# Optimization experiments

Measured on AMD Instinct MI355X. Metric: run time of the kernel, lower is better.

## Reference

```python
import jax, jax.numpy as jnp
import numpy as np

NHEAD = 8
DMODEL = 512
DK = DMODEL // NHEAD  # 64

def setup_inputs() -> dict:
    key = jax.random.key(0)
    ks = jax.random.split(key, 7)
    B, S = 4, 2048
    Q = jax.random.normal(ks[0], (B, S, DMODEL), dtype=jnp.float32)
    K = jax.random.normal(ks[1], (B, S, DMODEL), dtype=jnp.float32)
    V = jax.random.normal(ks[2], (B, S, DMODEL), dtype=jnp.float32)
    # Original uses torch.rand (uniform [0,1)) for all weights.
    WQ = jax.random.uniform(ks[3], (NHEAD, DMODEL, DK), dtype=jnp.float32)
    WK = jax.random.uniform(ks[4], (NHEAD, DMODEL, DK), dtype=jnp.float32)
    WV = jax.random.uniform(ks[5], (NHEAD, DMODEL, DK), dtype=jnp.float32)
    WO = jax.random.uniform(ks[6], (NHEAD * DK, DMODEL), dtype=jnp.float32)
    return {"Q": Q, "K": K, "V": V, "WQ": WQ, "WK": WK, "WV": WV, "WO": WO}

def reference(Q, K, V, WQ, WK, WV, WO):
    # Stacked per-head projections: [B,H,S,dk]
    Qh = jnp.einsum('bsd,hdk->bhsk', Q, WQ)
    Kh = jnp.einsum('bsd,hdk->bhsk', K, WK)
    Vh = jnp.einsum('bsd,hdk->bhsk', V, WV)
    dk = Kh.shape[-1]
    scores = jnp.einsum('bhqk,bhsk->bhqs', Qh, Kh) / jnp.sqrt(jnp.float32(dk))
    attn = jax.nn.softmax(scores, axis=-1)  # dropout omitted (eval / deterministic baseline)
    out = jnp.einsum('bhqs,bhsk->bhqk', attn, Vh)
    B, H, S, Dk = out.shape
    out = out.transpose(0, 2, 1, 3).reshape(B, S, H * Dk)  # concat heads on last dim
    return out @ WO
```

## Files before the change

kernel.cpp:

```cpp
#include <hip/hip_runtime.h>

#define NB 4
#define NS 2048
#define ND 512
#define NH 8
#define NDK 64

typedef __attribute__((ext_vector_type(8))) short bf16x8;
typedef __attribute__((ext_vector_type(4))) short bf16x4;
typedef __attribute__((ext_vector_type(4))) float f32x4;
typedef __attribute__((ext_vector_type(4))) int   i32x4;

__device__ inline f32x4 mfma16(bf16x8 a, bf16x8 b, f32x4 c) {
    return __builtin_amdgcn_mfma_f32_16x16x32_bf16(a, b, c, 0, 0, 0);
}
__device__ inline unsigned short f2bf(float f) {
    unsigned u = __float_as_uint(f);
    unsigned r = u + 0x7FFFu + ((u >> 16) & 1u);
    return (unsigned short)(r >> 16);
}
__device__ inline float bf2f(unsigned short h) {
    return __uint_as_float(((unsigned)h) << 16);
}
__device__ inline void splitf(float x, short& hi, short& lo) {
    unsigned short h = f2bf(x);
    hi = (short)h;
    lo = (short)f2bf(x - bf2f(h));
}
__device__ inline float exp2_fast(float x) {
    float r; asm("v_exp_f32 %0, %1" : "=v"(r) : "v"(x)); return r;
}

__global__ __launch_bounds__(256) void prep_split(
    const float* __restrict__ X, short* __restrict__ xh, short* __restrict__ xl)
{
    int i = (blockIdx.x * 256 + threadIdx.x) * 4;
    float4 f = *(const float4*)(X + i);
    short h0,h1,h2,h3,l0,l1,l2,l3;
    splitf(f.x,h0,l0); splitf(f.y,h1,l1); splitf(f.z,h2,l2); splitf(f.w,h3,l3);
    bf16x4 hv = {h0,h1,h2,h3}, lv = {l0,l1,l2,l3};
    *(bf16x4*)(xh + i) = hv;
    *(bf16x4*)(xl + i) = lv;
}

__global__ __launch_bounds__(256) void proj_kernel(
    const short* __restrict__ xqh, const short* __restrict__ xql,
    const short* __restrict__ xkh, const short* __restrict__ xkl,
    const float* __restrict__ Vf,
    const float* __restrict__ WQ, const float* __restrict__ WK,
    const float* __restrict__ WV,
    short* __restrict__ qth, short* __restrict__ qtl,
    short* __restrict__ kth, short* __restrict__ ktl,
    short* __restrict__ vt, int zbase)
{
    const int z = zbase + blockIdx.z;
    const int m0 = blockIdx.x * 128;
    const int h  = blockIdx.y;
    const int tid = threadIdx.x;
    const int w = tid >> 6, lane = tid & 63, c = lane & 15, g = lane >> 4;

    const short* xh = (z == 0) ? xqh : xkh;
    const short* xl = (z == 0) ? xql : xkl;
    const float* Wp = ((z == 0) ? WQ : (z == 1) ? WK : WV) + (size_t)h * ND * NDK;
    short* o1 = (z == 0) ? qth : (z == 1) ? kth : vt;
    short* o2 = (z == 0) ? qtl : ktl;

    __shared__ __align__(16) short smem[15360];
    short* sxh = smem;
    short* sxl = smem + 5120;
    short* swh = smem + 10240;
    short* swl = smem + 12800;

    f32x4 acc[2][4];
    #pragma unroll
    for (int i = 0; i < 2; i++)
        #pragma unroll
        for (int j = 0; j < 4; j++) acc[i][j] = f32x4{0.f,0.f,0.f,0.f};

    const int r_ = tid >> 1, kq = (tid & 1) * 16;
    const int kr0 = (tid*2) >> 4,     c40 = ((tid*2) & 15) * 4;
    const int kr1 = (tid*2+1) >> 4,   c41 = ((tid*2+1) & 15) * 4;

    bf16x8 rh0, rh1, rl0, rl1;
    float4 rv0, rv1, rv2, rv3;
    float4 rw0, rw1;

    auto LDX = [&](int k0) {
        if (z < 2) {
            const short* s1 = xh + (size_t)(m0 + r_) * ND + k0 + kq;
            const short* s2 = xl + (size_t)(m0 + r_) * ND + k0 + kq;
            rh0 = *(const bf16x8*)s1; rh1 = *(const bf16x8*)(s1 + 8);
            rl0 = *(const bf16x8*)s2; rl1 = *(const bf16x8*)(s2 + 8);
        } else {
            const float* s1 = Vf + (size_t)(m0 + r_) * ND + k0 + kq;
            rv0 = ((const float4*)s1)[0]; rv1 = ((const float4*)s1)[1];
            rv2 = ((const float4*)s1)[2]; rv3 = ((const float4*)s1)[3];
        }
    };
    auto LDW = [&](int k0) {
        rw0 = *(const float4*)(Wp + (size_t)(k0 + kr0) * NDK + c40);
        rw1 = *(const float4*)(Wp + (size_t)(k0 + kr1) * NDK + c41);
    };

    LDX(0); LDW(0);

    for (int k0 = 0; k0 < ND; k0 += 32) {
        if (z < 2) {
            *(bf16x8*)&sxh[r_*40 + kq]     = rh0;
            *(bf16x8*)&sxh[r_*40 + kq + 8] = rh1;
            *(bf16x8*)&sxl[r_*40 + kq]     = rl0;
            *(bf16x8*)&sxl[r_*40 + kq + 8] = rl1;
            short hh, ll;
            splitf(rw0.x, hh, ll); swh[(c40+0)*40 + kr0] = hh; swl[(c40+0)*40 + kr0] = ll;
            splitf(rw0.y, hh, ll); swh[(c40+1)*40 + kr0] = hh; swl[(c40+1)*40 + kr0] = ll;
            splitf(rw0.z, hh, ll); swh[(c40+2)*40 + kr0] = hh; swl[(c40+2)*40 + kr0] = ll;
            splitf(rw0.w, hh, ll); swh[(c40+3)*40 + kr0] = hh; swl[(c40+3)*40 + kr0] = ll;
            splitf(rw1.x, hh, ll); swh[(c41+0)*40 + kr1] = hh; swl[(c41+0)*40 + kr1] = ll;
            splitf(rw1.y, hh, ll); swh[(c41+1)*40 + kr1] = hh; swl[(c41+1)*40 + kr1] = ll;
            splitf(rw1.z, hh, ll); swh[(c41+2)*40 + kr1] = hh; swl[(c41+2)*40 + kr1] = ll;
            splitf(rw1.w, hh, ll); swh[(c41+3)*40 + kr1] = hh; swl[(c41+3)*40 + kr1] = ll;
        } else {
            short tmp[16];
            tmp[0]=(short)f2bf(rv0.x); tmp[1]=(short)f2bf(rv0.y);
            tmp[2]=(short)f2bf(rv0.z); tmp[3]=(short)f2bf(rv0.w);
            tmp[4]=(short)f2bf(rv1.x); tmp[5]=(short)f2bf(rv1.y);
            tmp[6]=(short)f2bf(rv1.z); tmp[7]=(short)f2bf(rv1.w);
            tmp[8]=(short)f2bf(rv2.x); tmp[9]=(short)f2bf(rv2.y);
            tmp[10]=(short)f2bf(rv2.z); tmp[11]=(short)f2bf(rv2.w);
            tmp[12]=(short)f2bf(rv3.x); tmp[13]=(short)f2bf(rv3.y);
            tmp[14]=(short)f2bf(rv3.z); tmp[15]=(short)f2bf(rv3.w);
            bf16x8 v0, v1;
            #pragma unroll
            for (int j = 0; j < 8; j++) { v0[j] = tmp[j]; v1[j] = tmp[8+j]; }
            *(bf16x8*)&sxh[r_*40 + kq]     = v0;
            *(bf16x8*)&sxh[r_*40 + kq + 8] = v1;
            swh[(c40+0)*40 + kr0] = (short)f2bf(rw0.x);
            swh[(c40+1)*40 + kr0] = (short)f2bf(rw0.y);
            swh[(c40+2)*40 + kr0] = (short)f2bf(rw0.z);
            swh[(c40+3)*40 + kr0] = (short)f2bf(rw0.w);
            swh[(c41+0)*40 + kr1] = (short)f2bf(rw1.x);
            swh[(c41+1)*40 + kr1] = (short)f2bf(rw1.y);
            swh[(c41+2)*40 + kr1] = (short)f2bf(rw1.z);
            swh[(c41+3)*40 + kr1] = (short)f2bf(rw1.w);
        }
        __syncthreads();

        if (k0 + 32 < ND) { LDX(k0 + 32); LDW(k0 + 32); }

        bf16x8 ah0 = *(bf16x8*)&sxh[(32*w +      c)*40 + 8*g];
        bf16x8 ah1 = *(bf16x8*)&sxh[(32*w + 16 + c)*40 + 8*g];
        bf16x8 al0, al1;
        if (z < 2) {
            al0 = *(bf16x8*)&sxl[(32*w +      c)*40 + 8*g];
            al1 = *(bf16x8*)&sxl[(32*w + 16 + c)*40 + 8*g];
        }
        #pragma unroll
        for (int nf = 0; nf < 4; nf++) {
            bf16x8 bh = *(bf16x8*)&swh[(c + 16*nf)*40 + 8*g];
            acc[0][nf] = mfma16(ah0, bh, acc[0][nf]);
            acc[1][nf] = mfma16(ah1, bh, acc[1][nf]);
            if (z < 2) {
                bf16x8 bl = *(bf16x8*)&swl[(c + 16*nf)*40 + 8*g];
                acc[0][nf] = mfma16(ah0, bl, acc[0][nf]);
                acc[1][nf] = mfma16(ah1, bl, acc[1][nf]);
                acc[0][nf] = mfma16(al0, bh, acc[0][nf]);
                acc[1][nf] = mfma16(al1, bh, acc[1][nf]);
            }
        }
        __syncthreads();
    }

    const int bh = (m0 >> 11) * NH + h;
    if (z < 2) {
        short* ep = smem;
        #pragma unroll
        for (int pass = 0; pass < 2; pass++) {
            __syncthreads();
            #pragma unroll
            for (int mi = 0; mi < 2; mi++)
                #pragma unroll
                for (int nf = 0; nf < 4; nf++)
                    #pragma unroll
                    for (int r = 0; r < 4; r++) {
                        int rl = 32*w + 16*mi + 4*g + r;
                        short hh, ll; splitf(acc[mi][nf][r], hh, ll);
                        ep[rl*72 + c + 16*nf] = pass ? ll : hh;
                    }
            __syncthreads();
            int rl = tid >> 1, half = tid & 1;
            int s = (m0 & 2047) + rl;
            int t = s >> 6, sr = s & 63;
            char* op = (char*)(pass ? o2 : o1) + ((size_t)bh * 32 + t) * 8192 + sr * 128;
            int sw = (sr & 7) << 4;
            #pragma unroll
            for (int ch = 0; ch < 4; ch++) {
                bf16x8 vv = *(bf16x8*)&ep[rl*72 + half*32 + ch*8];
                *(bf16x8*)(op + ((half*64 + ch*16) ^ sw)) = vv;
            }
        }
    } else {
        short* ep = smem;
        __syncthreads();
        #pragma unroll
        for (int mi = 0; mi < 2; mi++)
            #pragma unroll
            for (int nf = 0; nf < 4; nf++)
                #pragma unroll
                for (int r = 0; r < 4; r++) {
                    int rl = 32*w + 16*mi + 4*g + r;
                    ep[rl*72 + c + 16*nf] = (short)f2bf(acc[mi][nf][r]);
                }
        __syncthreads();
        int dk = tid >> 2, scq = (tid & 3) * 32;
        #pragma unroll
        for (int ch = 0; ch < 4; ch++) {
            int sl = scq + ch*8;
            int s = (m0 & 2047) + sl;
            int t = s >> 6, sr0 = s & 63;
            bf16x8 vv;
            #pragma unroll
            for (int i = 0; i < 8; i++) vv[i] = ep[(sl + i)*72 + dk];
            char* op = (char*)o1 + ((size_t)bh * 32 + t) * 8192 + dk * 128;
            *(bf16x8*)(op + ((2*sr0) ^ ((dk & 7) << 4))) = vv;
        }
    }
}

__global__ __launch_bounds__(256, 4) void attn_kernel(
    const short* __restrict__ qth, const short* __restrict__ qtl,
    const short* __restrict__ kth, const short* __restrict__ ktl,
    const short* __restrict__ vtl, short* __restrict__ ao)
{
    const int orig = blockIdx.x;
    const int wg = (orig & 7) * 128 + (orig >> 3);
    const int bh = wg >> 5, qb = (wg & 31) * 64;
    const int tid = threadIdx.x;
    const int w = tid >> 6, lane = tid & 63, c = lane & 15, g = lane >> 4;

    __shared__ __align__(16) short kh_s[64*64];
    __shared__ __align__(16) short kl_s[64*64];
    __shared__ __align__(16) short v_s [64*64];
    __shared__ __align__(16) short pb  [4][16*64];
    char* khb = (char*)kh_s;
    char* klb = (char*)kl_s;
    char* vb  = (char*)v_s;
    char* pwb = (char*)pb[w];
    short* pw = pb[w];

    bf16x8 qh[2], ql[2];
    {
        const char* qtbh = (const char*)qth + ((size_t)bh*32 + (qb>>6))*8192;
        const char* qtbl = (const char*)qtl + ((size_t)bh*32 + (qb>>6))*8192;
        int s_in = 16*w + c;
        int sw = (s_in & 7) << 4;
        qh[0] = *(const bf16x8*)(qtbh + s_in*128 + ((16*g) ^ sw));
        qh[1] = *(const bf16x8*)(qtbh + s_in*128 + ((64 + 16*g) ^ sw));
        ql[0] = *(const bf16x8*)(qtbl + s_in*128 + ((16*g) ^ sw));
        ql[1] = *(const bf16x8*)(qtbl + s_in*128 + ((64 + 16*g) ^ sw));
    }

    const char* kg = (const char*)kth + (size_t)bh * 262144;
    const char* lg = (const char*)ktl + (size_t)bh * 262144;
    const char* vg = (const char*)vtl + (size_t)bh * 262144;
    const int thr = w * 2048 + lane * 16;

    const float SC = 0.18033688f;
    float mrow[4], lrowp[4];
    f32x4 acc[4];
    #pragma unroll
    for (int r = 0; r < 4; r++) { mrow[r] = -1e30f; lrowp[r] = 0.f; }
    #pragma unroll
    for (int nf = 0; nf < 4; nf++) acc[nf] = f32x4{0.f,0.f,0.f,0.f};

    i32x4 s0, s1, s2, s3, s4, s5;
    {
        const char* p = kg + thr; s0 = *(const i32x4*)p; s1 = *(const i32x4*)(p + 1024);
        p = lg + thr;             s2 = *(const i32x4*)p; s3 = *(const i32x4*)(p + 1024);
        p = vg + thr;             s4 = *(const i32x4*)p; s5 = *(const i32x4*)(p + 1024);
    }

    for (int t = 0; t < 32; ++t) {
        {
            char* d = khb + thr; *(i32x4*)d = s0; *(i32x4*)(d + 1024) = s1;
            d = klb + thr;       *(i32x4*)d = s2; *(i32x4*)(d + 1024) = s3;
            d = vb + thr;        *(i32x4*)d = s4; *(i32x4*)(d + 1024) = s5;
        }
        __syncthreads();
        if (t < 31) {
            size_t off = (size_t)(t + 1) * 8192 + thr;
            const char* p = kg + off; s0 = *(const i32x4*)p; s1 = *(const i32x4*)(p + 1024);
            p = lg + off;             s2 = *(const i32x4*)p; s3 = *(const i32x4*)(p + 1024);
            p = vg + off;             s4 = *(const i32x4*)p; s5 = *(const i32x4*)(p + 1024);
        }

        f32x4 s4c[4];
        #pragma unroll
        for (int sf = 0; sf < 4; sf++) {
            s4c[sf] = f32x4{0.f,0.f,0.f,0.f};
            int rowK = c + 16*sf;
            #pragma unroll
            for (int ks = 0; ks < 2; ks++) {
                int cb = (ks*64 + 16*g) ^ ((rowK & 7) << 4);
                bf16x8 kh = *(bf16x8*)(khb + rowK*128 + cb);
                bf16x8 kl = *(bf16x8*)(klb + rowK*128 + cb);
                s4c[sf] = mfma16(qh[ks], kh, s4c[sf]);
                s4c[sf] = mfma16(qh[ks], kl, s4c[sf]);
                s4c[sf] = mfma16(ql[ks], kh, s4c[sf]);
            }
        }

        float tmax[4];
        #pragma unroll
        for (int r = 0; r < 4; r++) {
            float v = fmaxf(fmaxf(s4c[0][r], s4c[1][r]), fmaxf(s4c[2][r], s4c[3][r]));
            #pragma unroll
            for (int off = 1; off < 16; off <<= 1) v = fmaxf(v, __shfl_xor(v, off));
            tmax[r] = v;
        }
        float dmax = fmaxf(fmaxf(tmax[0]-mrow[0], tmax[1]-mrow[1]),
                           fmaxf(tmax[2]-mrow[2], tmax[3]-mrow[3]));
        if (!__all(dmax < -144.0f)) {
            if (__any(dmax > 64.0f)) {
                #pragma unroll
                for (int r = 0; r < 4; r++) {
                    float mn = fmaxf(mrow[r], tmax[r]);
                    float fc = exp2_fast((mrow[r] - mn) * SC);
                    mrow[r] = mn; lrowp[r] *= fc;
                    acc[0][r] *= fc; acc[1][r] *= fc; acc[2][r] *= fc; acc[3][r] *= fc;
                }
            }
            float mS[4];
            #pragma unroll
            for (int r = 0; r < 4; r++) mS[r] = mrow[r] * SC;
            float rs[4] = {0.f, 0.f, 0.f, 0.f};
            #pragma unroll
            for (int sf = 0; sf < 4; sf++) {
                #pragma unroll
                for (int r = 0; r < 4; r++) {
                    float p = exp2_fast(fmaf(s4c[sf][r], SC, -mS[r]));
                    rs[r] += p;
                    int q = 4*g + r;
                    *(short*)(pwb + q*128 + ((2*c + 32*sf) ^ ((q & 7) << 4))) =
                        (short)(__float_as_uint(p) >> 16);
                }
            }
            #pragma unroll
            for (int r = 0; r < 4; r++) lrowp[r] += rs[r];

            #pragma unroll
            for (int ks = 0; ks < 2; ks++) {
                int cbp = (ks*64 + 16*g) ^ ((c & 7) << 4);
                bf16x8 pa = *(bf16x8*)(pwb + c*128 + cbp);
                #pragma unroll
                for (int nf = 0; nf < 4; nf++) {
                    int rowV = c + 16*nf;
                    int cbv = (ks*64 + 16*g) ^ ((rowV & 7) << 4);
                    bf16x8 vv = *(bf16x8*)(vb + rowV*128 + cbv);
                    acc[nf] = mfma16(pa, vv, acc[nf]);
                }
            }
        }
        __syncthreads();
    }

    float inv[4];
    #pragma unroll
    for (int r = 0; r < 4; r++) {
        float t2 = lrowp[r];
        #pragma unroll
        for (int off = 1; off < 16; off <<= 1) t2 += __shfl_xor(t2, off);
        inv[r] = 1.f / t2;
    }
    #pragma unroll
    for (int nf = 0; nf < 4; nf++)
        #pragma unroll
        for (int r = 0; r < 4; r++)
            pw[(4*g + r)*64 + c + 16*nf] = (short)f2bf(acc[nf][r] * inv[r]);

    const int b = bh >> 3, hh = bh & 7;
    {
        int q = qb + 16*w + c;
        size_t o = ((size_t)b * NS + q) * ND + hh * NDK + g * 16;
        const short* src = pw + c*64 + g*16;
        *(bf16x8*)&ao[o]     = *(const bf16x8*)src;
        *(bf16x8*)&ao[o + 8] = *(const bf16x8*)(src + 8);
    }
}

__global__ __launch_bounds__(256) void oproj_kernel(
    const short* __restrict__ ao, const float* __restrict__ WO, float* __restrict__ out)
{
    const int orig = blockIdx.x;
    const int wg = (orig & 7) * 64 + (orig >> 3);
    const int mb = (wg >> 3) * 128, nb = (wg & 7) * 64;
    const int tid = threadIdx.x;
    const int w = tid >> 6, lane = tid & 63, c = lane & 15, g = lane >> 4;

    __shared__ __align__(16) short xlds[128*40];
    __shared__ __align__(16) short wt[64*40];

    f32x4 acc[2][4];
    #pragma unroll
    for (int i = 0; i < 2; i++)
        #pragma unroll
        for (int j = 0; j < 4; j++) acc[i][j] = f32x4{0.f,0.f,0.f,0.f};

    for (int k0 = 0; k0 < ND; k0 += 32) {
        {
            int r = tid >> 1, kq = (tid & 1) * 16;
            const short* src = ao + (size_t)(mb + r) * ND + k0 + kq;
            *(bf16x8*)&xlds[r*40 + kq]     = *(const bf16x8*)src;
            *(bf16x8*)&xlds[r*40 + kq + 8] = *(const bf16x8*)(src + 8);
        }
        #pragma unroll
        for (int i = 0; i < 2; i++) {
            int idx = tid * 2 + i;
            int kr = idx >> 4, c4 = (idx & 15) * 4;
            float4 f = *(const float4*)&WO[(size_t)(k0 + kr) * ND + nb + c4];
            wt[(c4+0)*40 + kr] = (short)f2bf(f.x);
            wt[(c4+1)*40 + kr] = (short)f2bf(f.y);
            wt[(c4+2)*40 + kr] = (short)f2bf(f.z);
            wt[(c4+3)*40 + kr] = (short)f2bf(f.w);
        }
        __syncthreads();
        bf16x8 a0 = *(bf16x8*)&xlds[(32*w +      c)*40 + 8*g];
        bf16x8 a1 = *(bf16x8*)&xlds[(32*w + 16 + c)*40 + 8*g];
        #pragma unroll
        for (int nf = 0; nf < 4; nf++) {
            bf16x8 bv = *(bf16x8*)&wt[(c + 16*nf)*40 + 8*g];
            acc[0][nf] = mfma16(a0, bv, acc[0][nf]);
            acc[1][nf] = mfma16(a1, bv, acc[1][nf]);
        }
        __syncthreads();
    }
    #pragma unroll
    for (int mi = 0; mi < 2; mi++)
        #pragma unroll
        for (int nf = 0; nf < 4; nf++)
            #pragma unroll
            for (int r = 0; r < 4; r++) {
                int row = mb + 32*w + 16*mi + 4*g + r;
                out[(size_t)row * ND + nb + c + 16*nf] = acc[mi][nf][r];
            }
}

extern "C" void kernel_launch(void* const* d_in, const int* in_sizes, int n_in,
                              void* d_out, int out_size, void* d_ws, size_t ws_size,
                              hipStream_t stream) {
    (void)in_sizes; (void)n_in; (void)out_size;
    const float* Q  = (const float*)d_in[0];
    const float* K  = (const float*)d_in[1];
    const float* V  = (const float*)d_in[2];
    const float* WQ = (const float*)d_in[3];
    const float* WK = (const float*)d_in[4];
    const float* WV = (const float*)d_in[5];
    const float* WO = (const float*)d_in[6];

    char* ws = (char*)d_ws;
    const size_t PLANE = (size_t)NB * NH * NS * NDK * 2;
    #define P(i) ((short*)(ws + (size_t)(i) * PLANE))

    if (ws_size >= 9 * PLANE) {
        short *xqh=P(0), *xql=P(1), *xkh=P(2), *xkl=P(3);
        short *qth=P(4), *qtl=P(5), *kth=P(6), *ktl=P(7), *vt=P(8);
        short *ao = P(0);
        prep_split<<<4096, 256, 0, stream>>>(Q, xqh, xql);
        prep_split<<<4096, 256, 0, stream>>>(K, xkh, xkl);
        proj_kernel<<<dim3(64, NH, 3), 256, 0, stream>>>(
            xqh, xql, xkh, xkl, V, WQ, WK, WV, qth, qtl, kth, ktl, vt, 0);
        attn_kernel<<<1024, 256, 0, stream>>>(qth, qtl, kth, ktl, vt, ao);
        oproj_kernel<<<512, 256, 0, stream>>>(ao, WO, (float*)d_out);
    } else {
        short *xh=P(0), *xl=P(1);
        short *qth=P(2), *qtl=P(3), *kth=P(4), *ktl=P(5);
        short *vt=P(0), *ao=P(1);
        prep_split<<<4096, 256, 0, stream>>>(Q, xh, xl);
        proj_kernel<<<dim3(64, NH, 1), 256, 0, stream>>>(
            xh, xl, xh, xl, V, WQ, WK, WV, qth, qtl, kth, ktl, vt, 0);
        prep_split<<<4096, 256, 0, stream>>>(K, xh, xl);
        proj_kernel<<<dim3(64, NH, 1), 256, 0, stream>>>(
            xh, xl, xh, xl, V, WQ, WK, WV, qth, qtl, kth, ktl, vt, 1);
        proj_kernel<<<dim3(64, NH, 1), 256, 0, stream>>>(
            xh, xl, xh, xl, V, WQ, WK, WV, qth, qtl, kth, ktl, vt, 2);
        attn_kernel<<<1024, 256, 0, stream>>>(qth, qtl, kth, ktl, vt, ao);
        oproj_kernel<<<512, 256, 0, stream>>>(ao, WO, (float*)d_out);
    }
    #undef P
}
```

Baseline: 295.9 us.

## Fuse activation split into projection, pre-split weights, widen tiles, add MFMA priority

Removes the separate prep_split passes over Q and K. The projection kernel now reads fp32 activations directly and splits them into bf16 hi/lo in registers. The weights are pre-split and transposed once by a small prep_w kernel into a scratch area inside the output buffer, and the projection tile grows to 128x128 (two heads per block) with a 4x4 accumulator per wave. s_setprio is also raised around the MFMA sections of attention. The aim is to cut global traffic and launches, at the cost of higher register use and a dependency on the output buffer being free until the final kernel overwrites it.

```diff
diff --git a/kernel.cpp b/kernel.cpp
--- a/kernel.cpp
+++ b/kernel.cpp
@@ -31,197 +31,200 @@
     float r; asm("v_exp_f32 %0, %1" : "=v"(r) : "v"(x)); return r;
 }
 
-__global__ __launch_bounds__(256) void prep_split(
-    const float* __restrict__ X, short* __restrict__ xh, short* __restrict__ xl)
-{
-    int i = (blockIdx.x * 256 + threadIdx.x) * 4;
-    float4 f = *(const float4*)(X + i);
-    short h0,h1,h2,h3,l0,l1,l2,l3;
-    splitf(f.x,h0,l0); splitf(f.y,h1,l1); splitf(f.z,h2,l2); splitf(f.w,h3,l3);
-    bf16x4 hv = {h0,h1,h2,h3}, lv = {l0,l1,l2,l3};
-    *(bf16x4*)(xh + i) = hv;
-    *(bf16x4*)(xl + i) = lv;
-}
-
-__global__ __launch_bounds__(256) void proj_kernel(
-    const short* __restrict__ xqh, const short* __restrict__ xql,
-    const short* __restrict__ xkh, const short* __restrict__ xkl,
-    const float* __restrict__ Vf,
+__global__ __launch_bounds__(256) void prep_w(
     const float* __restrict__ WQ, const float* __restrict__ WK,
     const float* __restrict__ WV,
+    short* __restrict__ wqh, short* __restrict__ wql,
+    short* __restrict__ wkh, short* __restrict__ wkl, short* __restrict__ wv)
+{
+    const int z = blockIdx.y;
+    const int gid = blockIdx.x * 256 + threadIdx.x;
+    const int idx = gid * 4;
+    const int dk = idx & 63;
+    const int d  = (idx >> 6) & 511;
+    const int h  = idx >> 15;
+    const float* src = ((z == 0) ? WQ : (z == 1) ? WK : WV) + idx;
+    float4 f = *(const float4*)src;
+    size_t o = (size_t)(h * 64 + dk) * 512 + d;
+    if (z < 2) {
+        short* oh = z ? wkh : wqh;
+        short* ol = z ? wkl : wql;
+        short hh, ll;
+        splitf(f.x, hh, ll); oh[o]        = hh; ol[o]        = ll;
+        splitf(f.y, hh, ll); oh[o +  512] = hh; ol[o +  512] = ll;
+        splitf(f.z, hh, ll); oh[o + 1024] = hh; ol[o + 1024] = ll;
+        splitf(f.w, hh, ll); oh[o + 1536] = hh; ol[o + 1536] = ll;
+    } else {
+        wv[o]        = (short)f2bf(f.x);
+        wv[o +  512] = (short)f2bf(f.y);
+        wv[o + 1024] = (short)f2bf(f.z);
+        wv[o + 1536] = (short)f2bf(f.w);
+    }
+}
+
+__global__ __launch_bounds__(256, 2) void proj(
+    const float* __restrict__ Q, const float* __restrict__ K,
+    const float* __restrict__ V,
+    const short* __restrict__ wqh, const short* __restrict__ wql,
+    const short* __restrict__ wkh, const short* __restrict__ wkl,
+    const short* __restrict__ wvp,
     short* __restrict__ qth, short* __restrict__ qtl,
-    short* __restrict__ kth, short* __restrict__ ktl,
-    short* __restrict__ vt, int zbase)
+    short* __restrict__ kth, short* __restrict__ ktl, short* __restrict__ vt)
 {
-    const int z = zbase + blockIdx.z;
+    const int z  = blockIdx.z;
     const int m0 = blockIdx.x * 128;
-    const int h  = blockIdx.y;
+    const int nb = blockIdx.y * 128;
     const int tid = threadIdx.x;
     const int w = tid >> 6, lane = tid & 63, c = lane & 15, g = lane >> 4;
-
-    const short* xh = (z == 0) ? xqh : xkh;
-    const short* xl = (z == 0) ? xql : xkl;
-    const float* Wp = ((z == 0) ? WQ : (z == 1) ? WK : WV) + (size_t)h * ND * NDK;
-    short* o1 = (z == 0) ? qth : (z == 1) ? kth : vt;
-    short* o2 = (z == 0) ? qtl : ktl;
-
-    __shared__ __align__(16) short smem[15360];
+    const int wm = w >> 1, wn = w & 1;
+
+    const float* X  = (z == 0) ? Q : (z == 1) ? K : V;
+    const short* Wh = (z == 0) ? wqh : (z == 1) ? wkh : wvp;
+    const short* Wl = (z == 0) ? wql : wkl;
+
+    __shared__ __align__(16) short smem[20480];
     short* sxh = smem;
     short* sxl = smem + 5120;
     short* swh = smem + 10240;
-    short* swl = smem + 12800;
-
-    f32x4 acc[2][4];
-    #pragma unroll
-    for (int i = 0; i < 2; i++)
-        #pragma unroll
-        for (int j = 0; j < 4; j++) acc[i][j] = f32x4{0.f,0.f,0.f,0.f};
+    short* swl = smem + 15360;
+
+    f32x4 acc[4][4];
+    #pragma unroll
+    for (int i = 0; i < 4; i++)
+        #pragma unroll
+        for (int j = 0; j < 4; j++) acc[i][j] = f32x4{0.f, 0.f, 0.f, 0.f};
 
     const int r_ = tid >> 1, kq = (tid & 1) * 16;
-    const int kr0 = (tid*2) >> 4,     c40 = ((tid*2) & 15) * 4;
-    const int kr1 = (tid*2+1) >> 4,   c41 = ((tid*2+1) & 15) * 4;
-
-    bf16x8 rh0, rh1, rl0, rl1;
-    float4 rv0, rv1, rv2, rv3;
-    float4 rw0, rw1;
-
-    auto LDX = [&](int k0) {
+
+    bf16x8 axh0, axh1, axl0, axl1;
+    bf16x8 awh0, awh1, awl0, awl1;
+
+    auto LD = [&](int k0) {
+        const float* s1 = X + (size_t)(m0 + r_) * ND + k0 + kq;
+        float4 f0 = ((const float4*)s1)[0];
+        float4 f1 = ((const float4*)s1)[1];
+        float4 f2 = ((const float4*)s1)[2];
+        float4 f3 = ((const float4*)s1)[3];
+        float xv[16] = {f0.x,f0.y,f0.z,f0.w, f1.x,f1.y,f1.z,f1.w,
+                        f2.x,f2.y,f2.z,f2.w, f3.x,f3.y,f3.z,f3.w};
+        short hv[16], lv[16];
         if (z < 2) {
-            const short* s1 = xh + (size_t)(m0 + r_) * ND + k0 + kq;
-            const short* s2 = xl + (size_t)(m0 + r_) * ND + k0 + kq;
-            rh0 = *(const bf16x8*)s1; rh1 = *(const bf16x8*)(s1 + 8);
-            rl0 = *(const bf16x8*)s2; rl1 = *(const bf16x8*)(s2 + 8);
+            #pragma unroll
+            for (int j = 0; j < 16; j++) splitf(xv[j], hv[j], lv[j]);
         } else {
-            const float* s1 = Vf + (size_t)(m0 + r_) * ND + k0 + kq;
-            rv0 = ((const float4*)s1)[0]; rv1 = ((const float4*)s1)[1];
-            rv2 = ((const float4*)s1)[2]; rv3 = ((const float4*)s1)[3];
+            #pragma unroll
+            for (int j = 0; j < 16; j++) hv[j] = (short)f2bf(xv[j]);
+        }
+        #pragma unroll
+        for (int j = 0; j < 8; j++) {
+            axh0[j] = hv[j]; axh1[j] = hv[8 + j];
+            if (z < 2) { axl0[j] = lv[j]; axl1[j] = lv[8 + j]; }
+        }
+        const short* ws1 = Wh + (size_t)(nb + r_) * ND + k0 + kq;
+        awh0 = *(const bf16x8*)ws1; awh1 = *(const bf16x8*)(ws1 + 8);
+        if (z < 2) {
+            const short* ws2 = Wl + (size_t)(nb + r_) * ND + k0 + kq;
+            awl0 = *(const bf16x8*)ws2; awl1 = *(const bf16x8*)(ws2 + 8);
         }
     };
-    auto LDW = [&](int k0) {
-        rw0 = *(const float4*)(Wp + (size_t)(k0 + kr0) * NDK + c40);
-        rw1 = *(const float4*)(Wp + (size_t)(k0 + kr1) * NDK + c41);
-    };
-
-    LDX(0); LDW(0);
+
+    LD(0);
 
     for (int k0 = 0; k0 < ND; k0 += 32) {
+        *(bf16x8*)&sxh[r_*40 + kq]     = axh0;
+        *(bf16x8*)&sxh[r_*40 + kq + 8] = axh1;
+        *(bf16x8*)&swh[r_*40 + kq]     = awh0;
+        *(bf16x8*)&swh[r_*40 + kq + 8] = awh1;
         if (z < 2) {
-            *(bf16x8*)&sxh[r_*40 + kq]     = rh0;
-            *(bf16x8*)&sxh[r_*40 + kq + 8] = rh1;
-            *(bf16x8*)&sxl[r_*40 + kq]     = rl0;
-            *(bf16x8*)&sxl[r_*40 + kq + 8] = rl1;
-            short hh, ll;
-            splitf(rw0.x, hh, ll); swh[(c40+0)*40 + kr0] = hh; swl[(c40+0)*40 + kr0] = ll;
-            splitf(rw0.y, hh, ll); swh[(c40+1)*40 + kr0] = hh; swl[(c40+1)*40 + kr0] = ll;
-            splitf(rw0.z, hh, ll); swh[(c40+2)*40 + kr0] = hh; swl[(c40+2)*40 + kr0] = ll;
-            splitf(rw0.w, hh, ll); swh[(c40+3)*40 + kr0] = hh; swl[(c40+3)*40 + kr0] = ll;
-            splitf(rw1.x, hh, ll); swh[(c41+0)*40 + kr1] = hh; swl[(c41+0)*40 + kr1] = ll;
-            splitf(rw1.y, hh, ll); swh[(c41+1)*40 + kr1] = hh; swl[(c41+1)*40 + kr1] = ll;
-            splitf(rw1.z, hh, ll); swh[(c41+2)*40 + kr1] = hh; swl[(c41+2)*40 + kr1] = ll;
-            splitf(rw1.w, hh, ll); swh[(c41+3)*40 + kr1] = hh; swl[(c41+3)*40 + kr1] = ll;
-        } else {
-            short tmp[16];
-            tmp[0]=(short)f2bf(rv0.x); tmp[1]=(short)f2bf(rv0.y);
-            tmp[2]=(short)f2bf(rv0.z); tmp[3]=(short)f2bf(rv0.w);
-            tmp[4]=(short)f2bf(rv1.x); tmp[5]=(short)f2bf(rv1.y);
-            tmp[6]=(short)f2bf(rv1.z); tmp[7]=(short)f2bf(rv1.w);
-            tmp[8]=(short)f2bf(rv2.x); tmp[9]=(short)f2bf(rv2.y);
-            tmp[10]=(short)f2bf(rv2.z); tmp[11]=(short)f2bf(rv2.w);
-            tmp[12]=(short)f2bf(rv3.x); tmp[13]=(short)f2bf(rv3.y);
-            tmp[14]=(short)f2bf(rv3.z); tmp[15]=(short)f2bf(rv3.w);
-            bf16x8 v0, v1;
-            #pragma unroll
-            for (int j = 0; j < 8; j++) { v0[j] = tmp[j]; v1[j] = tmp[8+j]; }
-            *(bf16x8*)&sxh[r_*40 + kq]     = v0;
-            *(bf16x8*)&sxh[r_*40 + kq + 8] = v1;
-            swh[(c40+0)*40 + kr0] = (short)f2bf(rw0.x);
-            swh[(c40+1)*40 + kr0] = (short)f2bf(rw0.y);
-            swh[(c40+2)*40 + kr0] = (short)f2bf(rw0.z);
-            swh[(c40+3)*40 + kr0] = (short)f2bf(rw0.w);
-            swh[(c41+0)*40 + kr1] = (short)f2bf(rw1.x);
-            swh[(c41+1)*40 + kr1] = (short)f2bf(rw1.y);
-            swh[(c41+2)*40 + kr1] = (short)f2bf(rw1.z);
-            swh[(c41+3)*40 + kr1] = (short)f2bf(rw1.w);
-        }
-        __syncthreads();
-
-        if (k0 + 32 < ND) { LDX(k0 + 32); LDW(k0 + 32); }
-
-        bf16x8 ah0 = *(bf16x8*)&sxh[(32*w +      c)*40 + 8*g];
-        bf16x8 ah1 = *(bf16x8*)&sxh[(32*w + 16 + c)*40 + 8*g];
-        bf16x8 al0, al1;
-        if (z < 2) {
-            al0 = *(bf16x8*)&sxl[(32*w +      c)*40 + 8*g];
-            al1 = *(bf16x8*)&sxl[(32*w + 16 + c)*40 + 8*g];
+            *(bf16x8*)&sxl[r_*40 + kq]     = axl0;
+            *(bf16x8*)&sxl[r_*40 + kq + 8] = axl1;
+            *(bf16x8*)&swl[r_*40 + kq]     = awl0;
+            *(bf16x8*)&swl[r_*40 + kq + 8] = awl1;
+        }
+        __syncthreads();
+        if (k0 + 32 < ND) LD(k0 + 32);
+
+        bf16x8 ah[4], al[4];
+        #pragma unroll
+        for (int mi = 0; mi < 4; mi++) {
+            ah[mi] = *(bf16x8*)&sxh[(64*wm + 16*mi + c)*40 + 8*g];
+            if (z < 2) al[mi] = *(bf16x8*)&sxl[(64*wm + 16*mi + c)*40 + 8*g];
         }
         #pragma unroll
         for (int nf = 0; nf < 4; nf++) {
-            bf16x8 bh = *(bf16x8*)&swh[(c + 16*nf)*40 + 8*g];
-            acc[0][nf] = mfma16(ah0, bh, acc[0][nf]);
-            acc[1][nf] = mfma16(ah1, bh, acc[1][nf]);
+            bf16x8 bh = *(bf16x8*)&swh[(64*wn + 16*nf + c)*40 + 8*g];
             if (z < 2) {
-                bf16x8 bl = *(bf16x8*)&swl[(c + 16*nf)*40 + 8*g];
-                acc[0][nf] = mfma16(ah0, bl, acc[0][nf]);
-                acc[1][nf] = mfma16(ah1, bl, acc[1][nf]);
-                acc[0][nf] = mfma16(al0, bh, acc[0][nf]);
-                acc[1][nf] = mfma16(al1, bh, acc[1][nf]);
-            }
-        }
-        __syncthreads();
-    }
-
-    const int bh = (m0 >> 11) * NH + h;
+                bf16x8 bl = *(bf16x8*)&swl[(64*wn + 16*nf + c)*40 + 8*g];
+                #pragma unroll
+                for (int mi = 0; mi < 4; mi++) {
+                    acc[mi][nf] = mfma16(ah[mi], bh, acc[mi][nf]);
+                    acc[mi][nf] = mfma16(ah[mi], bl, acc[mi][nf]);
+                    acc[mi][nf] = mfma16(al[mi], bh, acc[mi][nf]);
+                }
+            } else {
+                #pragma unroll
+                for (int mi = 0; mi < 4; mi++)
+                    acc[mi][nf] = mfma16(ah[mi], bh, acc[mi][nf]);
+            }
+        }
+        __syncthreads();
+    }
+
+    const int bbase = (m0 >> 11) * NH;
+    const int sbase = m0 & 2047;
+    short* ep = smem;
     if (z < 2) {
-        short* ep = smem;
         #pragma unroll
         for (int pass = 0; pass < 2; pass++) {
             __syncthreads();
             #pragma unroll
-            for (int mi = 0; mi < 2; mi++)
+            for (int mi = 0; mi < 4; mi++)
                 #pragma unroll
                 for (int nf = 0; nf < 4; nf++)
                     #pragma unroll
                     for (int r = 0; r < 4; r++) {
-                        int rl = 32*w + 16*mi + 4*g + r;
+                        int rl  = 64*wm + 16*mi + 4*g + r;
+                        int col = 64*wn + 16*nf + c;
                         short hh, ll; splitf(acc[mi][nf][r], hh, ll);
-                        ep[rl*72 + c + 16*nf] = pass ? ll : hh;
+                        ep[rl*136 + col] = pass ? ll : hh;
                     }
             __syncthreads();
-            int rl = tid >> 1, half = tid & 1;
-            int s = (m0 & 2047) + rl;
-            int t = s >> 6, sr = s & 63;
-            char* op = (char*)(pass ? o2 : o1) + ((size_t)bh * 32 + t) * 8192 + sr * 128;
-            int sw = (sr & 7) << 4;
-            #pragma unroll
-            for (int ch = 0; ch < 4; ch++) {
-                bf16x8 vv = *(bf16x8*)&ep[rl*72 + half*32 + ch*8];
-                *(bf16x8*)(op + ((half*64 + ch*16) ^ sw)) = vv;
-            }
+            int rl2 = tid >> 1, half = tid & 1;
+            int head = blockIdx.y * 2 + half;
+            int s = sbase + rl2;
+            int t = s >> 6, sr = s & 63, sw2 = (sr & 7) << 4;
+            short* dst = pass ? (z ? ktl : qtl) : (z ? kth : qth);
+            char* base = (char*)dst + ((size_t)(bbase + head) * 32 + t) * 8192 + sr * 128;
+            const short* row = &ep[rl2*136 + half*64];
+            #pragma unroll
+            for (int ch = 0; ch < 8; ch++)
+                *(bf16x8*)(base + ((ch*16) ^ sw2)) = *(const bf16x8*)(row + ch*8);
         }
     } else {
-        short* ep = smem;
-        __syncthreads();
-        #pragma unroll
-        for (int mi = 0; mi < 2; mi++)
+        __syncthreads();
+        #pragma unroll
+        for (int mi = 0; mi < 4; mi++)
             #pragma unroll
             for (int nf = 0; nf < 4; nf++)
                 #pragma unroll
                 for (int r = 0; r < 4; r++) {
-                    int rl = 32*w + 16*mi + 4*g + r;
-                    ep[rl*72 + c + 16*nf] = (short)f2bf(acc[mi][nf][r]);
+                    int rl  = 64*wm + 16*mi + 4*g + r;
+                    int col = 64*wn + 16*nf + c;
+                    ep[rl*136 + col] = (short)f2bf(acc[mi][nf][r]);
                 }
         __syncthreads();
-        int dk = tid >> 2, scq = (tid & 3) * 32;
-        #pragma unroll
-        for (int ch = 0; ch < 4; ch++) {
-            int sl = scq + ch*8;
-            int s = (m0 & 2047) + sl;
-            int t = s >> 6, sr0 = s & 63;
+        int col = tid >> 1, tt = tid & 1;
+        int head = blockIdx.y * 2 + (col >> 6), dk = col & 63;
+        int s0_ = sbase + tt * 64;
+        int t = s0_ >> 6;
+        char* base = (char*)vt + ((size_t)(bbase + head) * 32 + t) * 8192 + dk * 128;
+        int sw2 = (dk & 7) << 4;
+        #pragma unroll
+        for (int ch = 0; ch < 8; ch++) {
             bf16x8 vv;
             #pragma unroll
-            for (int i = 0; i < 8; i++) vv[i] = ep[(sl + i)*72 + dk];
-            char* op = (char*)o1 + ((size_t)bh * 32 + t) * 8192 + dk * 128;
-            *(bf16x8*)(op + ((2*sr0) ^ ((dk & 7) << 4))) = vv;
+            for (int i = 0; i < 8; i++) vv[i] = ep[(tt*64 + ch*8 + i)*136 + col];
+            *(bf16x8*)(base + ((ch*16) ^ sw2)) = vv;
         }
     }
 }
@@ -294,6 +297,7 @@
         }
 
         f32x4 s4c[4];
+        __builtin_amdgcn_s_setprio(1);
         #pragma unroll
         for (int sf = 0; sf < 4; sf++) {
             s4c[sf] = f32x4{0.f,0.f,0.f,0.f};
@@ -308,6 +312,7 @@
                 s4c[sf] = mfma16(ql[ks], kh, s4c[sf]);
             }
         }
+        __builtin_amdgcn_s_setprio(0);
 
         float tmax[4];
         #pragma unroll
@@ -347,6 +352,7 @@
             #pragma unroll
             for (int r = 0; r < 4; r++) lrowp[r] += rs[r];
 
+            __builtin_amdgcn_s_setprio(1);
             #pragma unroll
             for (int ks = 0; ks < 2; ks++) {
                 int cbp = (ks*64 + 16*g) ^ ((c & 7) << 4);
@@ -359,6 +365,7 @@
                     acc[nf] = mfma16(pa, vv, acc[nf]);
                 }
             }
+            __builtin_amdgcn_s_setprio(0);
         }
         __syncthreads();
     }
@@ -447,7 +454,7 @@
 extern "C" void kernel_launch(void* const* d_in, const int* in_sizes, int n_in,
                               void* d_out, int out_size, void* d_ws, size_t ws_size,
                               hipStream_t stream) {
-    (void)in_sizes; (void)n_in; (void)out_size;
+    (void)in_sizes; (void)n_in; (void)out_size; (void)ws_size;
     const float* Q  = (const float*)d_in[0];
     const float* K  = (const float*)d_in[1];
     const float* V  = (const float*)d_in[2];
@@ -458,32 +465,22 @@
 
     char* ws = (char*)d_ws;
     const size_t PLANE = (size_t)NB * NH * NS * NDK * 2;
-    #define P(i) ((short*)(ws + (size_t)(i) * PLANE))
-
-    if (ws_size >= 9 * PLANE) {
-        short *xqh=P(0), *xql=P(1), *xkh=P(2), *xkl=P(3);
-        short *qth=P(4), *qtl=P(5), *kth=P(6), *ktl=P(7), *vt=P(8);
-        short *ao = P(0);
-        prep_split<<<4096, 256, 0, stream>>>(Q, xqh, xql);
-        prep_split<<<4096, 256, 0, stream>>>(K, xkh, xkl);
-        proj_kernel<<<dim3(64, NH, 3), 256, 0, stream>>>(
-            xqh, xql, xkh, xkl, V, WQ, WK, WV, qth, qtl, kth, ktl, vt, 0);
-        attn_kernel<<<1024, 256, 0, stream>>>(qth, qtl, kth, ktl, vt, ao);
-        oproj_kernel<<<512, 256, 0, stream>>>(ao, WO, (float*)d_out);
-    } else {
-        short *xh=P(0), *xl=P(1);
-        short *qth=P(2), *qtl=P(3), *kth=P(4), *ktl=P(5);
-        short *vt=P(0), *ao=P(1);
-        prep_split<<<4096, 256, 0, stream>>>(Q, xh, xl);
-        proj_kernel<<<dim3(64, NH, 1), 256, 0, stream>>>(
-            xh, xl, xh, xl, V, WQ, WK, WV, qth, qtl, kth, ktl, vt, 0);
-        prep_split<<<4096, 256, 0, stream>>>(K, xh, xl);
-        proj_kernel<<<dim3(64, NH, 1), 256, 0, stream>>>(
-            xh, xl, xh, xl, V, WQ, WK, WV, qth, qtl, kth, ktl, vt, 1);
-        proj_kernel<<<dim3(64, NH, 1), 256, 0, stream>>>(
-            xh, xl, xh, xl, V, WQ, WK, WV, qth, qtl, kth, ktl, vt, 2);
-        attn_kernel<<<1024, 256, 0, stream>>>(qth, qtl, kth, ktl, vt, ao);
-        oproj_kernel<<<512, 256, 0, stream>>>(ao, WO, (float*)d_out);
-    }
-    #undef P
-}
+    short* qth = (short*)(ws);
+    short* qtl = (short*)(ws +     PLANE);
+    short* kth = (short*)(ws + 2 * PLANE);
+    short* ktl = (short*)(ws + 3 * PLANE);
+    short* vt  = (short*)(ws + 4 * PLANE);
+    short* ao  = (short*)(ws + 5 * PLANE);
+
+    short* wqh = (short*)d_out;
+    short* wql = wqh + 262144;
+    short* wkh = wqh + 2 * 262144;
+    short* wkl = wqh + 3 * 262144;
+    short* wv  = wqh + 4 * 262144;
+
+    prep_w<<<dim3(256, 3), 256, 0, stream>>>(WQ, WK, WV, wqh, wql, wkh, wkl, wv);
+    proj<<<dim3(64, 4, 3), 256, 0, stream>>>(Q, K, V, wqh, wql, wkh, wkl, wv,
+                                             qth, qtl, kth, ktl, vt);
+    attn_kernel<<<1024, 256, 0, stream>>>(qth, qtl, kth, ktl, vt, ao);
+    oproj_kernel<<<512, 256, 0, stream>>>(ao, WO, (float*)d_out);
+}
```

Measured after the change: 274.4 us. 7.3% less time.
